# Kernel optimization log

Measured on AMD Instinct MI355X. Metric: run time of the kernel, lower is better.

Reference implementation:

```python
import jax, jax.numpy as jnp
import numpy as np

ALPHA = 0.2
BETA = 1.0
TEMPERATURE = 0.05
EPS = 1e-8  # torch cosine_similarity eps


def setup_inputs() -> dict:
    key = jax.random.key(0)
    k1, k2 = jax.random.split(key)
    B, R, D = 4096, 18, 256  # rows, segment size (1 anchor + 1 pos + 16 negs), embed dim
    features = jax.random.normal(k1, (B * R, D), dtype=jnp.float32)
    scores = jax.random.normal(k2, (B * (R - 1),), dtype=jnp.float32)
    row_sizes = jnp.full((B,), R, dtype=jnp.int32)  # uniform ragged sizes
    logit_scale = jnp.array([1.0 / TEMPERATURE], dtype=jnp.float32)
    return {"features": features, "scores": scores, "row_sizes": row_sizes,
            "logit_scale": logit_scale}


def reference(features, scores, row_sizes, logit_scale):
    B = row_sizes.shape[0]
    R = features.shape[0] // B  # uniform segment size
    D = features.shape[1]
    f3 = features.reshape(B, R, D)
    anchor = f3[:, 0]          # [B, D]
    tgt = f3[:, 1:]            # [B, R-1, D]  (positive first, then negatives)

    # --- per-row cosine sims + log_softmax + KLDiv(batchmean) ---
    an = jnp.maximum(jnp.linalg.norm(anchor, axis=-1, keepdims=True), EPS)  # [B,1]
    tn = jnp.maximum(jnp.linalg.norm(tgt, axis=-1), EPS)                    # [B,R-1]
    cos = jnp.einsum('bd,bkd->bk', anchor, tgt) / (an * tn)                 # [B,R-1]
    emb_log = jax.nn.log_softmax(cos, axis=-1)                              # [B,R-1]
    ce = jax.nn.softmax(scores.reshape(B, R - 1), axis=-1)                  # [B,R-1]
    # torch KLDivLoss(reduction='batchmean') on a length-(R-1) vector divides by (R-1)
    kl = jnp.sum(ce * (jnp.log(ce) - emb_log), axis=-1) / (R - 1)           # [B]
    loss = jnp.mean(BETA * kl)

    # --- single InfoNCE over all rows: anchors vs [positives; all negatives] ---
    pos = f3[:, 1]                                   # [B, D]
    negs = f3[:, 2:].reshape(B * (R - 2), D)         # [B*(R-2), D]
    targets = jnp.concatenate([pos, negs], axis=0)   # [B*(R-1), D]
    logits = logit_scale[0] * (anchor @ targets.T)   # [B, B*(R-1)]
    labels = jnp.arange(B)
    # cross_entropy(logits, labels) with mean reduction
    infonce = jnp.mean(jax.nn.logsumexp(logits, axis=-1) - logits[labels, labels])

    return loss + ALPHA * infonce
```

## Files before the change

### kernel.cpp

```cpp
#include <hip/hip_runtime.h>
#include <math.h>

#define ALPHA 0.2f
#define BETA 1.0f
#define EPSV 1e-8f
#define LOG2E 1.4426950408889634f
#define LN2 0.6931471805599453f

#define BATCH 4096
#define RR 18
#define KT 17
#define DD 256
#define NTGT (BATCH*KT)

#define BMW 64
#define NWAVES 4
#define BMB (BMW*NWAVES)
#define MBLK (BATCH/BMB)
#define BN 64
#define NSPLIT 136
#define NSLOT NSPLIT
#define NSLICE (NTGT/NSPLIT)
#define NCHUNK (NSLICE/BN)
#define CHUNK_BYTES (BN*DD)

#define EXPA 8388608.0f
#define EXPB 1064880320.0f

typedef int   i32x8  __attribute__((ext_vector_type(8)));
typedef float f32x16 __attribute__((ext_vector_type(16)));

__device__ inline void gl_lds16(const void* g, void* l){
  __builtin_amdgcn_global_load_lds(
      (const __attribute__((address_space(1))) unsigned int*)g,
      (__attribute__((address_space(3))) unsigned int*)l, 16, 0, 0);
}

__device__ inline int pk8(float a, float b, float c, float d){
  int p = __builtin_amdgcn_cvt_pk_fp8_f32(a, b, 0, false);
  return  __builtin_amdgcn_cvt_pk_fp8_f32(c, d, p, true);
}

__device__ inline float fmax3(float a, float b, float c){
  return fmaxf(fmaxf(a, b), c);
}

__device__ inline float fexp2u(float x, float kc){
  float t = fmaf(x, EXPA, kc);
  unsigned u;
  asm("v_cvt_u32_f32 %0, %1" : "=v"(u) : "v"(t));
  return __uint_as_float(u);
}


__global__ __launch_bounds__(256) void prep_kernel(
    const float* __restrict__ feat, const float* __restrict__ scores,
    const float* __restrict__ lscale,
    unsigned char* __restrict__ abf8, unsigned char* __restrict__ tbf8,
    float* __restrict__ diag, float* __restrict__ klarr){
  __shared__ float csh[KT];
  int b = blockIdx.x, tid = threadIdx.x;
  int grp = tid >> 4, j = tid & 15;
  const float* fb = feat + (size_t)b * RR * DD;
  float s2 = lscale[0] * LOG2E;

  float4 a0 = ((const float4*)fb)[j*4+0];
  float4 a1 = ((const float4*)fb)[j*4+1];
  float4 a2 = ((const float4*)fb)[j*4+2];
  float4 a3 = ((const float4*)fb)[j*4+3];
  float asq = (a0.x*a0.x+a0.y*a0.y+a0.z*a0.z+a0.w*a0.w)
            + (a1.x*a1.x+a1.y*a1.y+a1.z*a1.z+a1.w*a1.w)
            + (a2.x*a2.x+a2.y*a2.y+a2.z*a2.z+a2.w*a2.w)
            + (a3.x*a3.x+a3.y*a3.y+a3.z*a3.z+a3.w*a3.w);
  #pragma unroll
  for (int off=1; off<16; off<<=1) asq += __shfl_xor(asq, off);
  float an = fmaxf(sqrtf(asq), EPSV);

  if (tid < 16){
    uint4 v = make_uint4(
      (unsigned)pk8(a0.x*s2,a0.y*s2,a0.z*s2,a0.w*s2),
      (unsigned)pk8(a1.x*s2,a1.y*s2,a1.z*s2,a1.w*s2),
      (unsigned)pk8(a2.x*s2,a2.y*s2,a2.z*s2,a2.w*s2),
      (unsigned)pk8(a3.x*s2,a3.y*s2,a3.z*s2,a3.w*s2));
    *(uint4*)(abf8 + (size_t)b*DD + j*16) = v;
  }

  for (int kr = grp+1; kr <= KT; kr += 16){
    const float4* tp = (const float4*)(fb + (size_t)kr*DD) + j*4;
    float4 t0=tp[0], t1=tp[1], t2=tp[2], t3=tp[3];
    int t  = b*KT + (kr-1);
    int c  = t >> 6, r = t & 63, mt = (r >> 5) & 1, m = r & 31;
    int ki = j >> 2, hf = (j >> 1) & 1, w = j & 1;
    uint4 v = make_uint4(
      (unsigned)pk8(t0.x,t0.y,t0.z,t0.w), (unsigned)pk8(t1.x,t1.y,t1.z,t1.w),
      (unsigned)pk8(t2.x,t2.y,t2.z,t2.w), (unsigned)pk8(t3.x,t3.y,t3.z,t3.w));
    *(uint4*)(tbf8 + (size_t)c*CHUNK_BYTES + (size_t)((ki*2+mt)*2+w)*1024
              + hf*512 + m*16) = v;
    float d = (a0.x*t0.x+a0.y*t0.y+a0.z*t0.z+a0.w*t0.w)
            + (a1.x*t1.x+a1.y*t1.y+a1.z*t1.z+a1.w*t1.w)
            + (a2.x*t2.x+a2.y*t2.y+a2.z*t2.z+a2.w*t2.w)
            + (a3.x*t3.x+a3.y*t3.y+a3.z*t3.z+a3.w*t3.w);
    float q = (t0.x*t0.x+t0.y*t0.y+t0.z*t0.z+t0.w*t0.w)
            + (t1.x*t1.x+t1.y*t1.y+t1.z*t1.z+t1.w*t1.w)
            + (t2.x*t2.x+t2.y*t2.y+t2.z*t2.z+t2.w*t2.w)
            + (t3.x*t3.x+t3.y*t3.y+t3.z*t3.z+t3.w*t3.w);
    #pragma unroll
    for (int off=1; off<16; off<<=1){ d += __shfl_xor(d,off); q += __shfl_xor(q,off); }
    if (j == 0){
      csh[kr-1] = d / (an * fmaxf(sqrtf(q), EPSV));
      if (kr == 1) diag[b] = d;
    }
  }
  __syncthreads();

  if (tid < 64){
    bool act = tid < KT;
    float c  = act ? csh[tid] : -INFINITY;
    float sv = act ? scores[(size_t)b*KT + tid] : -INFINITY;
    float cm = c, sm = sv;
    #pragma unroll
    for (int off=1; off<64; off<<=1){
      cm = fmaxf(cm, __shfl_xor(cm, off));
      sm = fmaxf(sm, __shfl_xor(sm, off));
    }
    float ec = act ? __builtin_amdgcn_exp2f((c -cm)*LOG2E) : 0.f;
    float es = act ? __builtin_amdgcn_exp2f((sv-sm)*LOG2E) : 0.f;
    float cs = ec, ss = es;
    #pragma unroll
    for (int off=1; off<64; off<<=1){
      cs += __shfl_xor(cs, off);
      ss += __shfl_xor(ss, off);
    }
    float lse_c = cm + __logf(cs);
    float lse_s = sm + __logf(ss);
    float kt = 0.f;
    if (act){
      float lq = sv - lse_s;
      float lp = c  - lse_c;
      kt = __builtin_amdgcn_exp2f(lq*LOG2E)*(lq - lp);
    }
    #pragma unroll
    for (int off=1; off<64; off<<=1) kt += __shfl_xor(kt, off);
    if (tid == 0) klarr[b] = kt * (1.0f/KT);
  }
}

__global__ __launch_bounds__(256,3) void gemm_lse_kernel(
    const unsigned char* __restrict__ abf8, const unsigned char* __restrict__ tbf8,
    float* __restrict__ part_m, float* __restrict__ part_s){
  __shared__ __align__(16) unsigned char Bs[2][CHUNK_BYTES];
  const int tid  = threadIdx.x;
  const int lane = tid & 63;
  const int wave = tid >> 6;
  const int mb   = blockIdx.y;
  const int ns   = blockIdx.x;
  const int l31  = lane & 31;
  const int half = lane >> 5;

  const char* gbase = (const char*)tbf8 + (size_t)(ns*NCHUNK)*CHUNK_BYTES;
  auto stage = [&](int ch){
    const char* g = gbase + (size_t)ch*CHUNK_BYTES;
    char* l = (char*)Bs[ch & 1];
    #pragma unroll
    for (int j=0;j<4;++j){
      int off = j*4096 + tid*16;
      gl_lds16(g + off, l + off);
    }
  };

  stage(0);

  i32x8 af[2][4];
  {
    const unsigned char* ab = abf8 + (size_t)(mb*BMB + wave*BMW)*DD;
    #pragma unroll
    for (int nt=0;nt<2;++nt)
      #pragma unroll
      for (int ki=0;ki<4;++ki){
        const unsigned char* p = ab + (size_t)(nt*32+l31)*DD + ki*64 + half*32;
        uint4 lo = *(const uint4*)p;
        uint4 hi = *(const uint4*)(p+16);
        af[nt][ki] = (i32x8){(int)lo.x,(int)lo.y,(int)lo.z,(int)lo.w,
                             (int)hi.x,(int)hi.y,(int)hi.z,(int)hi.w};
      }
  }

  float run_m[2] = {-INFINITY,-INFINITY};
  float run_s[2] = {0.f,0.f};

  for (int ch=0; ch<NCHUNK; ++ch){
    __syncthreads();
    if (ch+1 < NCHUNK) stage(ch+1);

    const unsigned char* frag = &Bs[ch & 1][0] + lane*16;

    f32x16 acc[2][2];
    #pragma unroll
    for (int mt=0;mt<2;++mt)
      #pragma unroll
      for (int nt=0;nt<2;++nt)
        acc[mt][nt] = (f32x16)(0.f);

    #pragma unroll
    for (int ki=0;ki<4;++ki){
      i32x8 tf[2];
      #pragma unroll
      for (int mt=0;mt<2;++mt){
        uint4 lo = *(const uint4*)(frag + (size_t)((ki*2+mt)*2+0)*1024);
        uint4 hi = *(const uint4*)(frag + (size_t)((ki*2+mt)*2+1)*1024);
        tf[mt] = (i32x8){(int)lo.x,(int)lo.y,(int)lo.z,(int)lo.w,
                         (int)hi.x,(int)hi.y,(int)hi.z,(int)hi.w};
      }
      acc[0][0] = __builtin_amdgcn_mfma_scale_f32_32x32x64_f8f6f4(
                      tf[0], af[0][ki], acc[0][0], 0,0, 0,127, 0,127);
      acc[0][1] = __builtin_amdgcn_mfma_scale_f32_32x32x64_f8f6f4(
                      tf[0], af[1][ki], acc[0][1], 0,0, 0,127, 0,127);
      acc[1][0] = __builtin_amdgcn_mfma_scale_f32_32x32x64_f8f6f4(
                      tf[1], af[0][ki], acc[1][0], 0,0, 0,127, 0,127);
      acc[1][1] = __builtin_amdgcn_mfma_scale_f32_32x32x64_f8f6f4(
                      tf[1], af[1][ki], acc[1][1], 0,0, 0,127, 0,127);
    }

    #pragma unroll
    for (int nt=0;nt<2;++nt){
      f32x16 t = __builtin_elementwise_max(acc[0][nt], acc[1][nt]);
      float x0 = fmax3(t[0], t[1], t[2]);
      float x1 = fmax3(t[3], t[4], t[5]);
      float x2 = fmax3(t[6], t[7], t[8]);
      float x3 = fmax3(t[9], t[10], t[11]);
      float x4 = fmax3(t[12], t[13], t[14]);
      float mx = fmaxf(fmax3(x0,x1,x2), fmax3(x3,x4,t[15]));

      float kc = fmaf(mx, -EXPA, EXPB);
      float s0=0.f, s1=0.f, s2=0.f, s3=0.f;
      #pragma unroll
      for (int r=0;r<16;r+=4){
        s0 += fexp2u(acc[0][nt][r  ],kc) + fexp2u(acc[1][nt][r  ],kc);
        s1 += fexp2u(acc[0][nt][r+1],kc) + fexp2u(acc[1][nt][r+1],kc);
        s2 += fexp2u(acc[0][nt][r+2],kc) + fexp2u(acc[1][nt][r+2],kc);
        s3 += fexp2u(acc[0][nt][r+3],kc) + fexp2u(acc[1][nt][r+3],kc);
      }
      float sh = (s0+s1)+(s2+s3);

      float nm = fmaxf(run_m[nt], mx);
      run_s[nt] = run_s[nt]*__builtin_amdgcn_exp2f(run_m[nt]-nm)
                + sh*__builtin_amdgcn_exp2f(mx-nm);
      run_m[nt] = nm;
    }
  }

  #pragma unroll
  for (int nt=0;nt<2;++nt){
    float om = __shfl_xor(run_m[nt], 32);
    float os = __shfl_xor(run_s[nt], 32);
    float nm = fmaxf(run_m[nt], om);
    float S  = run_s[nt]*__builtin_amdgcn_exp2f(run_m[nt]-nm)
             + os*__builtin_amdgcn_exp2f(om-nm);
    if (half == 0){
      int gm = mb*BMB + wave*BMW + nt*32 + l31;
      part_m[(size_t)gm*NSLOT + ns] = nm;
      part_s[(size_t)gm*NSLOT + ns] = S;
    }
  }
}

__global__ __launch_bounds__(256) void combine_kernel(
    const float* __restrict__ part_m, const float* __restrict__ part_s,
    const float* __restrict__ diag, const float* __restrict__ lscale,
    float* __restrict__ infarr){
  int lane = threadIdx.x & 63, wave = threadIdx.x >> 6;
  int b = blockIdx.x*4 + wave;
  float s = lscale[0];
  const float* pm = part_m + (size_t)b*NSLOT;
  const float* ps = part_s + (size_t)b*NSLOT;
  float m = -INFINITY, S = 0.f;
  for (int i = lane; i < NSLOT; i += 64){
    float pm_ = pm[i], ps_ = ps[i];
    float nm = fmaxf(m, pm_);
    S = S*__builtin_amdgcn_exp2f(m-nm) + ps_*__builtin_amdgcn_exp2f(pm_-nm);
    m = nm;
  }
  #pragma unroll
  for (int off=1; off<64; off<<=1){
    float om = __shfl_xor(m, off), os = __shfl_xor(S, off);
    float nm = fmaxf(m, om);
    S = S*__builtin_amdgcn_exp2f(m-nm) + os*__builtin_amdgcn_exp2f(om-nm);
    m = nm;
  }
  if (lane == 0)
    infarr[b] = (m + __log2f(S))*LN2 - s*diag[b];
}

__global__ __launch_bounds__(256) void final_kernel(
    const float* __restrict__ infarr, const float* __restrict__ klarr,
    float* __restrict__ out){
  __shared__ float shi[4], shk[4];
  int tid = threadIdx.x, lane = tid & 63, wave = tid >> 6;
  float inf = 0.f, kl = 0.f;
  for (int i = tid; i < BATCH; i += 256){ inf += infarr[i]; kl += klarr[i]; }
  #pragma unroll
  for (int off=1; off<64; off<<=1){
    inf += __shfl_xor(inf, off);
    kl  += __shfl_xor(kl,  off);
  }
  if (lane == 0){ shi[wave] = inf; shk[wave] = kl; }
  __syncthreads();
  if (tid == 0){
    float I = shi[0]+shi[1]+shi[2]+shi[3];
    float K = shk[0]+shk[1]+shk[2]+shk[3];
    out[0] = BETA*(K*(1.0f/BATCH)) + ALPHA*(I*(1.0f/BATCH));
  }
}

extern "C" void kernel_launch(void* const* d_in, const int* in_sizes, int n_in,
                              void* d_out, int out_size, void* d_ws, size_t ws_size,
                              hipStream_t stream){
  const float* feat   = (const float*)d_in[0];
  const float* scores = (const float*)d_in[1];
  const float* lscale = (const float*)d_in[3];

  float* ws     = (float*)d_ws;
  float* diag   = ws;
  float* klarr  = diag + BATCH;
  float* infarr = klarr + BATCH;
  float* part_m = infarr + BATCH;
  float* part_s = part_m + (size_t)BATCH*NSLOT;
  unsigned char* abf8 = (unsigned char*)(part_s + (size_t)BATCH*NSLOT);
  unsigned char* tbf8 = abf8 + (size_t)BATCH*DD;

  prep_kernel<<<BATCH, 256, 0, stream>>>(feat, scores, lscale, abf8, tbf8, diag, klarr);
  gemm_lse_kernel<<<dim3(NSPLIT, MBLK), 256, 0, stream>>>(abf8, tbf8, part_m, part_s);
  combine_kernel<<<BATCH/4, 256, 0, stream>>>(part_m, part_s, diag, lscale, infarr);
  final_kernel<<<1, 256, 0, stream>>>(infarr, klarr, (float*)d_out);
}
```

Baseline: 204.7 us.

## Replace LDS-staged GEMM with single-wave register double-buffered tiles, fuse final reduction

The GEMM becomes a one-wave workgroup. Each wave loads 32-row FP8 target tiles straight from global memory into registers with double buffering, replacing the LDS staging through async global-to-LDS loads and the block barriers. The target layout changes to 32-row tiles and the split count drops from 136 to 32, so the combine step now reads only 32 partials per row, and block indices are swizzled to improve L2 locality. The final reduction kernel is dropped in favour of atomicAdd into an output that the prep kernel zeroes. In exchange there is less target-data reuse per workgroup, more L2 traffic, and more register pressure.

```diff
diff --git a/kernel.cpp b/kernel.cpp
--- a/kernel.cpp
+++ b/kernel.cpp
@@ -12,29 +12,18 @@
 #define KT 17
 #define DD 256
 #define NTGT (BATCH*KT)
-
-#define BMW 64
-#define NWAVES 4
-#define BMB (BMW*NWAVES)
-#define MBLK (BATCH/BMB)
-#define BN 64
-#define NSPLIT 136
-#define NSLOT NSPLIT
-#define NSLICE (NTGT/NSPLIT)
-#define NCHUNK (NSLICE/BN)
-#define CHUNK_BYTES (BN*DD)
+#define NTILE (NTGT/32)
+#define TILE_BYTES (32*DD)
+
+#define AG 64
+#define NSPLIT 32
+#define TPS (NTILE/NSPLIT)
 
 #define EXPA 8388608.0f
 #define EXPB 1064880320.0f
 
 typedef int   i32x8  __attribute__((ext_vector_type(8)));
 typedef float f32x16 __attribute__((ext_vector_type(16)));
-
-__device__ inline void gl_lds16(const void* g, void* l){
-  __builtin_amdgcn_global_load_lds(
-      (const __attribute__((address_space(1))) unsigned int*)g,
-      (__attribute__((address_space(3))) unsigned int*)l, 16, 0, 0);
-}
 
 __device__ inline int pk8(float a, float b, float c, float d){
   int p = __builtin_amdgcn_cvt_pk_fp8_f32(a, b, 0, false);
@@ -57,12 +46,15 @@
     const float* __restrict__ feat, const float* __restrict__ scores,
     const float* __restrict__ lscale,
     unsigned char* __restrict__ abf8, unsigned char* __restrict__ tbf8,
-    float* __restrict__ diag, float* __restrict__ klarr){
+    float* __restrict__ diag, float* __restrict__ klarr,
+    float* __restrict__ out){
   __shared__ float csh[KT];
   int b = blockIdx.x, tid = threadIdx.x;
   int grp = tid >> 4, j = tid & 15;
   const float* fb = feat + (size_t)b * RR * DD;
   float s2 = lscale[0] * LOG2E;
+
+  if (b == 0 && tid == 0) out[0] = 0.f;
 
   float4 a0 = ((const float4*)fb)[j*4+0];
   float4 a1 = ((const float4*)fb)[j*4+1];
@@ -89,13 +81,12 @@
     const float4* tp = (const float4*)(fb + (size_t)kr*DD) + j*4;
     float4 t0=tp[0], t1=tp[1], t2=tp[2], t3=tp[3];
     int t  = b*KT + (kr-1);
-    int c  = t >> 6, r = t & 63, mt = (r >> 5) & 1, m = r & 31;
+    int tile = t >> 5, m = t & 31;
     int ki = j >> 2, hf = (j >> 1) & 1, w = j & 1;
     uint4 v = make_uint4(
       (unsigned)pk8(t0.x,t0.y,t0.z,t0.w), (unsigned)pk8(t1.x,t1.y,t1.z,t1.w),
       (unsigned)pk8(t2.x,t2.y,t2.z,t2.w), (unsigned)pk8(t3.x,t3.y,t3.z,t3.w));
-    *(uint4*)(tbf8 + (size_t)c*CHUNK_BYTES + (size_t)((ki*2+mt)*2+w)*1024
-              + hf*512 + m*16) = v;
+    *(uint4*)(tbf8 + (size_t)tile*TILE_BYTES + ki*2048 + w*1024 + hf*512 + m*16) = v;
     float d = (a0.x*t0.x+a0.y*t0.y+a0.z*t0.z+a0.w*t0.w)
             + (a1.x*t1.x+a1.y*t1.y+a1.z*t1.z+a1.w*t1.w)
             + (a2.x*t2.x+a2.y*t2.y+a2.z*t2.z+a2.w*t2.w)
@@ -145,34 +136,19 @@
   }
 }
 
-__global__ __launch_bounds__(256,3) void gemm_lse_kernel(
+__global__ __launch_bounds__(64,2) void gemm_lse_kernel(
     const unsigned char* __restrict__ abf8, const unsigned char* __restrict__ tbf8,
     float* __restrict__ part_m, float* __restrict__ part_s){
-  __shared__ __align__(16) unsigned char Bs[2][CHUNK_BYTES];
-  const int tid  = threadIdx.x;
-  const int lane = tid & 63;
-  const int wave = tid >> 6;
-  const int mb   = blockIdx.y;
-  const int ns   = blockIdx.x;
+  const int bid  = blockIdx.x;
+  const int ns   = (bid & 7)*4 + ((bid >> 3) & 3);
+  const int ag   = bid >> 5;
+  const int lane = threadIdx.x;
   const int l31  = lane & 31;
   const int half = lane >> 5;
 
-  const char* gbase = (const char*)tbf8 + (size_t)(ns*NCHUNK)*CHUNK_BYTES;
-  auto stage = [&](int ch){
-    const char* g = gbase + (size_t)ch*CHUNK_BYTES;
-    char* l = (char*)Bs[ch & 1];
-    #pragma unroll
-    for (int j=0;j<4;++j){
-      int off = j*4096 + tid*16;
-      gl_lds16(g + off, l + off);
-    }
-  };
-
-  stage(0);
-
   i32x8 af[2][4];
   {
-    const unsigned char* ab = abf8 + (size_t)(mb*BMB + wave*BMW)*DD;
+    const unsigned char* ab = abf8 + (size_t)ag*64*DD;
     #pragma unroll
     for (int nt=0;nt<2;++nt)
       #pragma unroll
@@ -185,45 +161,43 @@
       }
   }
 
+  const unsigned char* gbase =
+      tbf8 + (size_t)(ns*TPS)*TILE_BYTES + half*512 + l31*16;
+
+  i32x8 ta[4], tb[4];
+  auto ld = [&](int tt, i32x8 tf[4]){
+    const unsigned char* p = gbase + (size_t)tt*TILE_BYTES;
+    #pragma unroll
+    for (int ki=0;ki<4;++ki){
+      uint4 lo = *(const uint4*)(p + ki*2048);
+      uint4 hi = *(const uint4*)(p + ki*2048 + 1024);
+      tf[ki] = (i32x8){(int)lo.x,(int)lo.y,(int)lo.z,(int)lo.w,
+                       (int)hi.x,(int)hi.y,(int)hi.z,(int)hi.w};
+    }
+  };
+
   float run_m[2] = {-INFINITY,-INFINITY};
   float run_s[2] = {0.f,0.f};
-
-  for (int ch=0; ch<NCHUNK; ++ch){
-    __syncthreads();
-    if (ch+1 < NCHUNK) stage(ch+1);
-
-    const unsigned char* frag = &Bs[ch & 1][0] + lane*16;
-
-    f32x16 acc[2][2];
-    #pragma unroll
-    for (int mt=0;mt<2;++mt)
-      #pragma unroll
-      for (int nt=0;nt<2;++nt)
-        acc[mt][nt] = (f32x16)(0.f);
-
+  f32x16 acc[2];
+
+  auto mfma_tile = [&](i32x8 tf[4]){
+    acc[0] = (f32x16)(0.f);
+    acc[1] = (f32x16)(0.f);
+    __builtin_amdgcn_s_setprio(1);
     #pragma unroll
     for (int ki=0;ki<4;++ki){
-      i32x8 tf[2];
-      #pragma unroll
-      for (int mt=0;mt<2;++mt){
-        uint4 lo = *(const uint4*)(frag + (size_t)((ki*2+mt)*2+0)*1024);
-        uint4 hi = *(const uint4*)(frag + (size_t)((ki*2+mt)*2+1)*1024);
-        tf[mt] = (i32x8){(int)lo.x,(int)lo.y,(int)lo.z,(int)lo.w,
-                         (int)hi.x,(int)hi.y,(int)hi.z,(int)hi.w};
-      }
-      acc[0][0] = __builtin_amdgcn_mfma_scale_f32_32x32x64_f8f6f4(
-                      tf[0], af[0][ki], acc[0][0], 0,0, 0,127, 0,127);
-      acc[0][1] = __builtin_amdgcn_mfma_scale_f32_32x32x64_f8f6f4(
-                      tf[0], af[1][ki], acc[0][1], 0,0, 0,127, 0,127);
-      acc[1][0] = __builtin_amdgcn_mfma_scale_f32_32x32x64_f8f6f4(
-                      tf[1], af[0][ki], acc[1][0], 0,0, 0,127, 0,127);
-      acc[1][1] = __builtin_amdgcn_mfma_scale_f32_32x32x64_f8f6f4(
-                      tf[1], af[1][ki], acc[1][1], 0,0, 0,127, 0,127);
-    }
-
+      acc[0] = __builtin_amdgcn_mfma_scale_f32_32x32x64_f8f6f4(
+                   tf[ki], af[0][ki], acc[0], 0,0, 0,127, 0,127);
+      acc[1] = __builtin_amdgcn_mfma_scale_f32_32x32x64_f8f6f4(
+                   tf[ki], af[1][ki], acc[1], 0,0, 0,127, 0,127);
+    }
+    __builtin_amdgcn_s_setprio(0);
+  };
+
+  auto epilogue = [&](){
     #pragma unroll
     for (int nt=0;nt<2;++nt){
-      f32x16 t = __builtin_elementwise_max(acc[0][nt], acc[1][nt]);
+      f32x16 t = acc[nt];
       float x0 = fmax3(t[0], t[1], t[2]);
       float x1 = fmax3(t[3], t[4], t[5]);
       float x2 = fmax3(t[6], t[7], t[8]);
@@ -235,10 +209,10 @@
       float s0=0.f, s1=0.f, s2=0.f, s3=0.f;
       #pragma unroll
       for (int r=0;r<16;r+=4){
-        s0 += fexp2u(acc[0][nt][r  ],kc) + fexp2u(acc[1][nt][r  ],kc);
-        s1 += fexp2u(acc[0][nt][r+1],kc) + fexp2u(acc[1][nt][r+1],kc);
-        s2 += fexp2u(acc[0][nt][r+2],kc) + fexp2u(acc[1][nt][r+2],kc);
-        s3 += fexp2u(acc[0][nt][r+3],kc) + fexp2u(acc[1][nt][r+3],kc);
+        s0 += fexp2u(t[r  ],kc);
+        s1 += fexp2u(t[r+1],kc);
+        s2 += fexp2u(t[r+2],kc);
+        s3 += fexp2u(t[r+3],kc);
       }
       float sh = (s0+s1)+(s2+s3);
 
@@ -247,6 +221,17 @@
                 + sh*__builtin_amdgcn_exp2f(mx-nm);
       run_m[nt] = nm;
     }
+  };
+
+  ld(0, ta);
+  ld(1, tb);
+  for (int t=0; t<TPS; t+=2){
+    mfma_tile(ta);
+    if (t+2 < TPS) ld(t+2, ta);
+    epilogue();
+    mfma_tile(tb);
+    if (t+3 < TPS) ld(t+3, tb);
+    epilogue();
   }
 
   #pragma unroll
@@ -257,59 +242,34 @@
     float S  = run_s[nt]*__builtin_amdgcn_exp2f(run_m[nt]-nm)
              + os*__builtin_amdgcn_exp2f(om-nm);
     if (half == 0){
-      int gm = mb*BMB + wave*BMW + nt*32 + l31;
-      part_m[(size_t)gm*NSLOT + ns] = nm;
-      part_s[(size_t)gm*NSLOT + ns] = S;
+      int gm = ag*64 + nt*32 + l31;
+      part_m[(size_t)ns*BATCH + gm] = nm;
+      part_s[(size_t)ns*BATCH + gm] = S;
     }
   }
 }
 
 __global__ __launch_bounds__(256) void combine_kernel(
     const float* __restrict__ part_m, const float* __restrict__ part_s,
-    const float* __restrict__ diag, const float* __restrict__ lscale,
-    float* __restrict__ infarr){
-  int lane = threadIdx.x & 63, wave = threadIdx.x >> 6;
-  int b = blockIdx.x*4 + wave;
+    const float* __restrict__ diag, const float* __restrict__ klarr,
+    const float* __restrict__ lscale, float* __restrict__ out){
+  int tid = threadIdx.x;
+  int b = blockIdx.x*256 + tid;
   float s = lscale[0];
-  const float* pm = part_m + (size_t)b*NSLOT;
-  const float* ps = part_s + (size_t)b*NSLOT;
   float m = -INFINITY, S = 0.f;
-  for (int i = lane; i < NSLOT; i += 64){
-    float pm_ = pm[i], ps_ = ps[i];
+  #pragma unroll
+  for (int ns=0; ns<NSPLIT; ++ns){
+    float pm_ = part_m[(size_t)ns*BATCH + b];
+    float ps_ = part_s[(size_t)ns*BATCH + b];
     float nm = fmaxf(m, pm_);
     S = S*__builtin_amdgcn_exp2f(m-nm) + ps_*__builtin_amdgcn_exp2f(pm_-nm);
     m = nm;
   }
-  #pragma unroll
-  for (int off=1; off<64; off<<=1){
-    float om = __shfl_xor(m, off), os = __shfl_xor(S, off);
-    float nm = fmaxf(m, om);
-    S = S*__builtin_amdgcn_exp2f(m-nm) + os*__builtin_amdgcn_exp2f(om-nm);
-    m = nm;
-  }
-  if (lane == 0)
-    infarr[b] = (m + __log2f(S))*LN2 - s*diag[b];
-}
-
-__global__ __launch_bounds__(256) void final_kernel(
-    const float* __restrict__ infarr, const float* __restrict__ klarr,
-    float* __restrict__ out){
-  __shared__ float shi[4], shk[4];
-  int tid = threadIdx.x, lane = tid & 63, wave = tid >> 6;
-  float inf = 0.f, kl = 0.f;
-  for (int i = tid; i < BATCH; i += 256){ inf += infarr[i]; kl += klarr[i]; }
-  #pragma unroll
-  for (int off=1; off<64; off<<=1){
-    inf += __shfl_xor(inf, off);
-    kl  += __shfl_xor(kl,  off);
-  }
-  if (lane == 0){ shi[wave] = inf; shk[wave] = kl; }
-  __syncthreads();
-  if (tid == 0){
-    float I = shi[0]+shi[1]+shi[2]+shi[3];
-    float K = shk[0]+shk[1]+shk[2]+shk[3];
-    out[0] = BETA*(K*(1.0f/BATCH)) + ALPHA*(I*(1.0f/BATCH));
-  }
+  float inf = (m + __log2f(S))*LN2 - s*diag[b];
+  float c = BETA*klarr[b] + ALPHA*inf;
+  #pragma unroll
+  for (int off=1; off<64; off<<=1) c += __shfl_xor(c, off);
+  if ((tid & 63) == 0) atomicAdd(out, c*(1.0f/BATCH));
 }
 
 extern "C" void kernel_launch(void* const* d_in, const int* in_sizes, int n_in,
@@ -322,14 +282,15 @@
   float* ws     = (float*)d_ws;
   float* diag   = ws;
   float* klarr  = diag + BATCH;
-  float* infarr = klarr + BATCH;
-  float* part_m = infarr + BATCH;
-  float* part_s = part_m + (size_t)BATCH*NSLOT;
-  unsigned char* abf8 = (unsigned char*)(part_s + (size_t)BATCH*NSLOT);
+  float* part_m = klarr + BATCH;
+  float* part_s = part_m + (size_t)NSPLIT*BATCH;
+  unsigned char* abf8 = (unsigned char*)(part_s + (size_t)NSPLIT*BATCH);
   unsigned char* tbf8 = abf8 + (size_t)BATCH*DD;
 
-  prep_kernel<<<BATCH, 256, 0, stream>>>(feat, scores, lscale, abf8, tbf8, diag, klarr);
-  gemm_lse_kernel<<<dim3(NSPLIT, MBLK), 256, 0, stream>>>(abf8, tbf8, part_m, part_s);
-  combine_kernel<<<BATCH/4, 256, 0, stream>>>(part_m, part_s, diag, lscale, infarr);
-  final_kernel<<<1, 256, 0, stream>>>(infarr, klarr, (float*)d_out);
-}
+  float* outp = (float*)d_out;
+  prep_kernel<<<BATCH, 256, 0, stream>>>(feat, scores, lscale, abf8, tbf8,
+                                         diag, klarr, outp);
+  gemm_lse_kernel<<<AG*NSPLIT, 64, 0, stream>>>(abf8, tbf8, part_m, part_s);
+  combine_kernel<<<BATCH/256, 256, 0, stream>>>(part_m, part_s, diag, klarr,
+                                                lscale, outp);
+}
```

After: 190.0 us. -7.2%, faster.
